# Performance work log

Measured on AMD Instinct MI355X. Metric: run time of the kernel, lower is better.

Reference implementation:

```python
import jax, jax.numpy as jnp
import numpy as np

N_NODES = 100000
N_EDGES = 1600000
D_IN = 64
D_HID = 64
D_OUT = 16


def setup_inputs() -> dict:
    key = jax.random.key(0)
    k1, k2, k3, k4 = jax.random.split(key, 4)
    x = jax.random.normal(k1, (N_NODES, D_IN), dtype=jnp.float32)
    edge_index = jax.random.randint(k2, (2, N_EDGES), 0, N_NODES, dtype=jnp.int64)
    # Glorot-ish scaled weights
    W1 = jax.random.normal(k3, (D_IN, D_HID), dtype=jnp.float32) / np.sqrt(D_IN)
    b1 = jnp.zeros((D_HID,), dtype=jnp.float32)
    W2 = jax.random.normal(k4, (D_HID, D_OUT), dtype=jnp.float32) / np.sqrt(D_HID)
    b2 = jnp.zeros((D_OUT,), dtype=jnp.float32)
    return {"x": x, "edge_index": edge_index, "W1": W1, "b1": b1, "W2": W2, "b2": b2}


def _gcn_conv(x, src, dst, W, b, n_nodes):
    """PyG GCNConv: D^{-1/2} (A + I) D^{-1/2} X W + b (self-loops added)."""
    h = x @ W  # [N, F_out]
    # degree including self-loop (counted on destination, PyG default)
    deg = jnp.zeros((n_nodes,), dtype=h.dtype).at[dst].add(1.0) + 1.0
    dinv = jax.lax.rsqrt(deg)  # deg >= 1, no inf
    # edge messages: norm_e = dinv[src] * dinv[dst]
    msg = h[src] * (dinv[src] * dinv[dst])[:, None]  # [E, F_out]
    out = jax.ops.segment_sum(msg, dst, num_segments=n_nodes)
    # self-loop contribution: norm = dinv[i]^2
    out = out + h * (dinv * dinv)[:, None]
    return out + b


def reference(x, edge_index, W1, b1, W2, b2):
    src, dst = edge_index[0], edge_index[1]
    n = x.shape[0]
    h = _gcn_conv(x, src, dst, W1, b1, n)
    h = jax.nn.relu(h)
    # F.dropout(training=False) at inference -> identity
    h = _gcn_conv(h, src, dst, W2, b2, n)
    return jax.nn.log_softmax(h, axis=1)
```

## Files before the change

kernel.cpp:

```cpp
#include <hip/hip_runtime.h>
#include <hip/hip_fp16.h>
#include <math.h>

#define N_NODES 100000
#define N_EDGES 1600000


__global__ void k_count(const int* __restrict__ dst, int* __restrict__ cnt,
                        unsigned short* __restrict__ rnk, int e) {
    int i = (blockIdx.x * blockDim.x + threadIdx.x) * 8;
    if (i + 8 <= e) {
        int4 dA = *(const int4*)(dst + i);
        int4 dB = *(const int4*)(dst + i + 4);
        int r0 = atomicAdd(&cnt[dA.x], 1);
        int r1 = atomicAdd(&cnt[dA.y], 1);
        int r2 = atomicAdd(&cnt[dA.z], 1);
        int r3 = atomicAdd(&cnt[dA.w], 1);
        int r4 = atomicAdd(&cnt[dB.x], 1);
        int r5 = atomicAdd(&cnt[dB.y], 1);
        int r6 = atomicAdd(&cnt[dB.z], 1);
        int r7 = atomicAdd(&cnt[dB.w], 1);
        int4 p;
        p.x = (r0 & 0xffff) | (r1 << 16);
        p.y = (r2 & 0xffff) | (r3 << 16);
        p.z = (r4 & 0xffff) | (r5 << 16);
        p.w = (r6 & 0xffff) | (r7 << 16);
        *(int4*)(rnk + i) = p;
    } else {
        for (; i < e; ++i) rnk[i] = (unsigned short)atomicAdd(&cnt[dst[i]], 1);
    }
}

__global__ void k_scanA(const int* __restrict__ cnt, int* __restrict__ off,
                        int* __restrict__ bsums, float* __restrict__ dinv, int n) {
    __shared__ int sd[256];
    int t = threadIdx.x;
    int base = blockIdx.x * 1024 + t * 4;
    int e0 = (base + 0 < n) ? cnt[base + 0] : 0;
    int e1 = (base + 1 < n) ? cnt[base + 1] : 0;
    int e2 = (base + 2 < n) ? cnt[base + 2] : 0;
    int e3 = (base + 3 < n) ? cnt[base + 3] : 0;
    if (base + 0 < n) dinv[base + 0] = rsqrtf((float)e0 + 1.0f);
    if (base + 1 < n) dinv[base + 1] = rsqrtf((float)e1 + 1.0f);
    if (base + 2 < n) dinv[base + 2] = rsqrtf((float)e2 + 1.0f);
    if (base + 3 < n) dinv[base + 3] = rsqrtf((float)e3 + 1.0f);
    int s = e0 + e1 + e2 + e3;
    sd[t] = s;
    __syncthreads();
    for (int o = 1; o < 256; o <<= 1) {
        int v = (t >= o) ? sd[t - o] : 0;
        __syncthreads();
        sd[t] += v;
        __syncthreads();
    }
    int excl = sd[t] - s;
    if (base + 0 < n) off[base + 0] = excl;
    if (base + 1 < n) off[base + 1] = excl + e0;
    if (base + 2 < n) off[base + 2] = excl + e0 + e1;
    if (base + 3 < n) off[base + 3] = excl + e0 + e1 + e2;
    if (t == 0) bsums[blockIdx.x] = sd[255];
}

__global__ void k_scanC(int* __restrict__ off, const int* __restrict__ bsums,
                        int nb, int n) {
    __shared__ int sd[128];
    int t = threadIdx.x;
    if (t < 128) sd[t] = (t < nb) ? bsums[t] : 0;
    __syncthreads();
    for (int o = 1; o < 128; o <<= 1) {
        int v = (t >= o && t < 128) ? sd[t - o] : 0;
        __syncthreads();
        if (t < 128) sd[t] += v;
        __syncthreads();
    }
    int i = blockIdx.x * 256 + t;
    if (i < n) {
        int b = i >> 10;
        int add = (b == 0) ? 0 : sd[b - 1];
        off[i] = off[i] + add;
    }
    if (blockIdx.x == 0 && t == 0) off[n] = sd[nb - 1];
}

__global__ void k_fill(const int* __restrict__ src, const int* __restrict__ dst,
                       const unsigned short* __restrict__ rnk,
                       const int* __restrict__ off, int* __restrict__ csr, int e) {
    int i = (blockIdx.x * blockDim.x + threadIdx.x) * 8;
    if (i + 8 <= e) {
        int4 sA = *(const int4*)(src + i), sB = *(const int4*)(src + i + 4);
        int4 dA = *(const int4*)(dst + i), dB = *(const int4*)(dst + i + 4);
        int4 rp = *(const int4*)(rnk + i);
        csr[off[dA.x] + (rp.x & 0xffff)] = sA.x;
        csr[off[dA.y] + ((unsigned)rp.x >> 16)] = sA.y;
        csr[off[dA.z] + (rp.y & 0xffff)] = sA.z;
        csr[off[dA.w] + ((unsigned)rp.y >> 16)] = sA.w;
        csr[off[dB.x] + (rp.z & 0xffff)] = sB.x;
        csr[off[dB.y] + ((unsigned)rp.z >> 16)] = sB.y;
        csr[off[dB.z] + (rp.w & 0xffff)] = sB.z;
        csr[off[dB.w] + ((unsigned)rp.w >> 16)] = sB.w;
    } else {
        for (; i < e; ++i) csr[off[dst[i]] + rnk[i]] = src[i];
    }
}

__global__ void k_fold(const float* __restrict__ x, const float* __restrict__ dinv,
                       float* __restrict__ xs) {
    int t = blockIdx.x * blockDim.x + threadIdx.x;
    float4 v = ((const float4*)x)[t];
    float di = dinv[t >> 4];
    float4 o;
    o.x = v.x * di; o.y = v.y * di; o.z = v.z * di; o.w = v.w * di;
    ((float4*)xs)[t] = o;
}


__global__ void k_agg1(
        const float* __restrict__ xs, const int* __restrict__ off,
        const int* __restrict__ csr, const float* __restrict__ dinv,
        const float* __restrict__ W1, const float* __restrict__ W2,
        const float* __restrict__ b1, __half* __restrict__ h2h, int n) {
    __shared__ float W1s[64 * 64];
    __shared__ float W2s[64 * 17];
    __shared__ float xsw[4][64];
    __shared__ float vsw[4][64];
    int tid = threadIdx.x;
    {
        const float4* W14 = (const float4*)W1;
        float4* W1s4 = (float4*)W1s;
#pragma unroll
        for (int i = 0; i < 4; ++i) W1s4[tid + 256 * i] = W14[tid + 256 * i];
        for (int i = tid; i < 64 * 16; i += 256) W2s[(i >> 4) * 17 + (i & 15)] = W2[i];
    }
    __syncthreads();

    int w = tid >> 6, lane = tid & 63;
    int f = lane;
    int G = lane >> 4;
    int c4 = lane & 15;
    float b1f = b1[f];

    int base = blockIdx.x * 16 + w * 4;
#pragma unroll 1
    for (int nn = 0; nn < 4; ++nn) {
        int d = base + nn;
        float dd = dinv[d];
        float a0 = xs[(size_t)d * 64 + f];
        float a1 = 0.f, a2 = 0.f, a3 = 0.f;
        int j = off[d], je = off[d + 1];
        int s0 = 0, s1 = 0, s2 = 0, s3 = 0;
        if (j + 4 <= je) { s0 = csr[j]; s1 = csr[j + 1]; s2 = csr[j + 2]; s3 = csr[j + 3]; }
        while (j + 4 <= je) {
            int t0 = s0, t1 = s1, t2 = s2, t3 = s3;
            if (j + 8 <= je) { t0 = csr[j + 4]; t1 = csr[j + 5]; t2 = csr[j + 6]; t3 = csr[j + 7]; }
            a0 += xs[(size_t)s0 * 64 + f];
            a1 += xs[(size_t)s1 * 64 + f];
            a2 += xs[(size_t)s2 * 64 + f];
            a3 += xs[(size_t)s3 * 64 + f];
            s0 = t0; s1 = t1; s2 = t2; s3 = t3;
            j += 4;
        }
        for (; j < je; ++j) {
            int s = csr[j];
            a0 += xs[(size_t)s * 64 + f];
        }
        xsw[w][f] = ((a0 + a1) + (a2 + a3)) * dd;
        float p0 = b1f, p1 = 0.f, p2 = 0.f, p3 = 0.f;
        const float4* xw4 = (const float4*)xsw[w];
#pragma unroll
        for (int k4 = 0; k4 < 16; ++k4) {
            float4 xv = xw4[k4];
            p0 = fmaf(xv.x, W1s[(k4 * 4 + 0) * 64 + f], p0);
            p1 = fmaf(xv.y, W1s[(k4 * 4 + 1) * 64 + f], p1);
            p2 = fmaf(xv.z, W1s[(k4 * 4 + 2) * 64 + f], p2);
            p3 = fmaf(xv.w, W1s[(k4 * 4 + 3) * 64 + f], p3);
        }
        vsw[w][f] = fmaxf((p0 + p1) + (p2 + p3), 0.f);
        float p = 0.f;
        const float4* vw4 = (const float4*)vsw[w];
#pragma unroll
        for (int kk4 = 0; kk4 < 4; ++kk4) {
            float4 vv = vw4[G * 4 + kk4];
            p = fmaf(vv.x, W2s[(G * 16 + kk4 * 4 + 0) * 17 + c4], p);
            p = fmaf(vv.y, W2s[(G * 16 + kk4 * 4 + 1) * 17 + c4], p);
            p = fmaf(vv.z, W2s[(G * 16 + kk4 * 4 + 2) * 17 + c4], p);
            p = fmaf(vv.w, W2s[(G * 16 + kk4 * 4 + 3) * 17 + c4], p);
        }
        p += __shfl_xor(p, 16);
        p += __shfl_xor(p, 32);
        if (G == 0) h2h[(size_t)d * 16 + c4] = __float2half(p * dd);
    }
}


__global__ void k_agg2_lsm(
        const __half* __restrict__ h2h, const int* __restrict__ off,
        const int* __restrict__ csr, const float* __restrict__ dinv,
        const float* __restrict__ b2, float* __restrict__ y, int n) {
    int tid = threadIdx.x;
    int w = tid >> 6, lane = tid & 63, g = lane >> 4, c = lane & 15;
    int d = blockIdx.x * 4 + w;
    float dd = dinv[d];
    float acc0 = (g == 0) ? __half2float(h2h[(size_t)d * 16 + c]) : 0.f;
    float acc1 = 0.f, acc2 = 0.f, acc3 = 0.f;
    int j = off[d], je = off[d + 1];
    for (; j + 16 <= je; j += 16) {
        int sA = csr[j + g], sB = csr[j + 4 + g];
        int sC = csr[j + 8 + g], sD = csr[j + 12 + g];
        acc0 += __half2float(h2h[(size_t)sA * 16 + c]);
        acc1 += __half2float(h2h[(size_t)sB * 16 + c]);
        acc2 += __half2float(h2h[(size_t)sC * 16 + c]);
        acc3 += __half2float(h2h[(size_t)sD * 16 + c]);
    }
    for (; j < je; j += 4) {
        if (j + g < je) {
            int s = csr[j + g];
            acc0 += __half2float(h2h[(size_t)s * 16 + c]);
        }
    }
    float acc = (acc0 + acc1) + (acc2 + acc3);
    acc += __shfl_xor(acc, 16);
    acc += __shfl_xor(acc, 32);
    float v = acc * dd + b2[c];
    float m = v;
#pragma unroll
    for (int o = 1; o < 16; o <<= 1) m = fmaxf(m, __shfl_xor(m, o));
    float ss = expf(v - m);
#pragma unroll
    for (int o = 1; o < 16; o <<= 1) ss += __shfl_xor(ss, o);
    float lse = logf(ss) + m;
    if (g == 0) y[(size_t)d * 16 + c] = v - lse;
}


extern "C" void kernel_launch(void* const* d_in, const int* in_sizes, int n_in,
                              void* d_out, int out_size, void* d_ws, size_t ws_size,
                              hipStream_t stream) {
    const float* x  = (const float*)d_in[0];
    const int*   ei = (const int*)d_in[1];
    const float* W1 = (const float*)d_in[2];
    const float* b1 = (const float*)d_in[3];
    const float* W2 = (const float*)d_in[4];
    const float* b2 = (const float*)d_in[5];
    float* y = (float*)d_out;

    const int n = N_NODES;
    const int e = N_EDGES;
    const int* src = ei;
    const int* dst = ei + e;

    float* ws = (float*)d_ws;
    int*            cnt   = (int*)ws;
    float*          dinv  = ws + 102400;
    int*            off   = (int*)(ws + 204800);
    int*            bsums = (int*)(ws + 307200);
    unsigned short* rnk   = (unsigned short*)(ws + 409600);
    int*            csr   = (int*)(ws + 1209600);
    float*          xs    = ws + 2809600;
    __half*         h2h   = (__half*)(ws + 9209600);

    const int nb = (n + 1023) / 1024;

    hipMemsetAsync(cnt, 0, (size_t)n * sizeof(int), stream);
    k_count<<<(e / 8 + 255) / 256, 256, 0, stream>>>(dst, cnt, rnk, e);
    k_scanA<<<nb, 256, 0, stream>>>(cnt, off, bsums, dinv, n);
    k_fold <<<n * 16 / 256, 256, 0, stream>>>(x, dinv, xs);
    k_scanC<<<(n + 255) / 256, 256, 0, stream>>>(off, bsums, nb, n);
    k_fill <<<(e / 8 + 255) / 256, 256, 0, stream>>>(src, dst, rnk, off, csr, e);

    k_agg1    <<<n / 16, 256, 0, stream>>>(xs, off, csr, dinv, W1, W2, b1, h2h, n);
    k_agg2_lsm<<<n / 4, 256, 0, stream>>>(h2h, off, csr, dinv, b2, y, n);
}
```

Baseline: 278.3 us.

## Fuse fold into fill kernel and vectorize layer-2 gather with half2

Merges the x-scaling fold kernel into the CSR fill kernel as extra blocks, recomputing dinv from the degree counts so it no longer depends on scanA's output. This removes one launch and lets the two independent memory-bound jobs run at the same time. The layer-2 aggregation now has each lane load half2 pairs with 8 lanes per row, so a wave processes 8 edges per step instead of 4. The output is also written as float2. Softmax shuffle reductions shrink to match the new lane layout.

```diff
diff --git a/kernel.cpp b/kernel.cpp
--- a/kernel.cpp
+++ b/kernel.cpp
@@ -82,35 +82,40 @@
     if (blockIdx.x == 0 && t == 0) off[n] = sd[nb - 1];
 }
 
-__global__ void k_fill(const int* __restrict__ src, const int* __restrict__ dst,
-                       const unsigned short* __restrict__ rnk,
-                       const int* __restrict__ off, int* __restrict__ csr, int e) {
-    int i = (blockIdx.x * blockDim.x + threadIdx.x) * 8;
-    if (i + 8 <= e) {
-        int4 sA = *(const int4*)(src + i), sB = *(const int4*)(src + i + 4);
-        int4 dA = *(const int4*)(dst + i), dB = *(const int4*)(dst + i + 4);
-        int4 rp = *(const int4*)(rnk + i);
-        csr[off[dA.x] + (rp.x & 0xffff)] = sA.x;
-        csr[off[dA.y] + ((unsigned)rp.x >> 16)] = sA.y;
-        csr[off[dA.z] + (rp.y & 0xffff)] = sA.z;
-        csr[off[dA.w] + ((unsigned)rp.y >> 16)] = sA.w;
-        csr[off[dB.x] + (rp.z & 0xffff)] = sB.x;
-        csr[off[dB.y] + ((unsigned)rp.z >> 16)] = sB.y;
-        csr[off[dB.z] + (rp.w & 0xffff)] = sB.z;
-        csr[off[dB.w] + ((unsigned)rp.w >> 16)] = sB.w;
+
+#define FILL_BLOCKS 782
+
+__global__ void k_fill_fold(const int* __restrict__ src, const int* __restrict__ dst,
+                            const unsigned short* __restrict__ rnk,
+                            const int* __restrict__ off, int* __restrict__ csr,
+                            const float* __restrict__ x, const int* __restrict__ cnt,
+                            float* __restrict__ xs, int e) {
+    int bid = blockIdx.x;
+    if (bid < FILL_BLOCKS) {
+        int i = (bid * blockDim.x + threadIdx.x) * 8;
+        if (i + 8 <= e) {
+            int4 sA = *(const int4*)(src + i), sB = *(const int4*)(src + i + 4);
+            int4 dA = *(const int4*)(dst + i), dB = *(const int4*)(dst + i + 4);
+            int4 rp = *(const int4*)(rnk + i);
+            csr[off[dA.x] + (rp.x & 0xffff)] = sA.x;
+            csr[off[dA.y] + ((unsigned)rp.x >> 16)] = sA.y;
+            csr[off[dA.z] + (rp.y & 0xffff)] = sA.z;
+            csr[off[dA.w] + ((unsigned)rp.y >> 16)] = sA.w;
+            csr[off[dB.x] + (rp.z & 0xffff)] = sB.x;
+            csr[off[dB.y] + ((unsigned)rp.z >> 16)] = sB.y;
+            csr[off[dB.z] + (rp.w & 0xffff)] = sB.z;
+            csr[off[dB.w] + ((unsigned)rp.w >> 16)] = sB.w;
+        } else {
+            for (; i < e; ++i) csr[off[dst[i]] + rnk[i]] = src[i];
+        }
     } else {
-        for (; i < e; ++i) csr[off[dst[i]] + rnk[i]] = src[i];
-    }
-}
-
-__global__ void k_fold(const float* __restrict__ x, const float* __restrict__ dinv,
-                       float* __restrict__ xs) {
-    int t = blockIdx.x * blockDim.x + threadIdx.x;
-    float4 v = ((const float4*)x)[t];
-    float di = dinv[t >> 4];
-    float4 o;
-    o.x = v.x * di; o.y = v.y * di; o.z = v.z * di; o.w = v.w * di;
-    ((float4*)xs)[t] = o;
+        int t = (bid - FILL_BLOCKS) * blockDim.x + threadIdx.x;
+        float4 v = ((const float4*)x)[t];
+        float di = rsqrtf((float)cnt[t >> 4] + 1.0f);
+        float4 o;
+        o.x = v.x * di; o.y = v.y * di; o.z = v.z * di; o.w = v.w * di;
+        ((float4*)xs)[t] = o;
+    }
 }
 
 
@@ -197,38 +202,47 @@
         const int* __restrict__ csr, const float* __restrict__ dinv,
         const float* __restrict__ b2, float* __restrict__ y, int n) {
     int tid = threadIdx.x;
-    int w = tid >> 6, lane = tid & 63, g = lane >> 4, c = lane & 15;
+    int w = tid >> 6, lane = tid & 63, g = lane >> 3, c2 = lane & 7;
     int d = blockIdx.x * 4 + w;
+    const __half2* h2 = (const __half2*)h2h;
     float dd = dinv[d];
-    float acc0 = (g == 0) ? __half2float(h2h[(size_t)d * 16 + c]) : 0.f;
-    float acc1 = 0.f, acc2 = 0.f, acc3 = 0.f;
+    float2 sv = __half22float2(h2[(size_t)d * 8 + c2]);
+    float ax0 = (g == 0) ? sv.x : 0.f;
+    float ay0 = (g == 0) ? sv.y : 0.f;
+    float ax1 = 0.f, ay1 = 0.f;
     int j = off[d], je = off[d + 1];
     for (; j + 16 <= je; j += 16) {
-        int sA = csr[j + g], sB = csr[j + 4 + g];
-        int sC = csr[j + 8 + g], sD = csr[j + 12 + g];
-        acc0 += __half2float(h2h[(size_t)sA * 16 + c]);
-        acc1 += __half2float(h2h[(size_t)sB * 16 + c]);
-        acc2 += __half2float(h2h[(size_t)sC * 16 + c]);
-        acc3 += __half2float(h2h[(size_t)sD * 16 + c]);
-    }
-    for (; j < je; j += 4) {
+        int sA = csr[j + g], sB = csr[j + 8 + g];
+        float2 vA = __half22float2(h2[(size_t)sA * 8 + c2]);
+        float2 vB = __half22float2(h2[(size_t)sB * 8 + c2]);
+        ax0 += vA.x; ay0 += vA.y;
+        ax1 += vB.x; ay1 += vB.y;
+    }
+    for (; j < je; j += 8) {
         if (j + g < je) {
             int s = csr[j + g];
-            acc0 += __half2float(h2h[(size_t)s * 16 + c]);
-        }
-    }
-    float acc = (acc0 + acc1) + (acc2 + acc3);
-    acc += __shfl_xor(acc, 16);
-    acc += __shfl_xor(acc, 32);
-    float v = acc * dd + b2[c];
-    float m = v;
-#pragma unroll
-    for (int o = 1; o < 16; o <<= 1) m = fmaxf(m, __shfl_xor(m, o));
-    float ss = expf(v - m);
-#pragma unroll
-    for (int o = 1; o < 16; o <<= 1) ss += __shfl_xor(ss, o);
+            float2 v = __half22float2(h2[(size_t)s * 8 + c2]);
+            ax0 += v.x; ay0 += v.y;
+        }
+    }
+    float ax = ax0 + ax1, ay = ay0 + ay1;
+    ax += __shfl_xor(ax, 8);  ax += __shfl_xor(ax, 16); ax += __shfl_xor(ax, 32);
+    ay += __shfl_xor(ay, 8);  ay += __shfl_xor(ay, 16); ay += __shfl_xor(ay, 32);
+    float vx = ax * dd + b2[c2 * 2 + 0];
+    float vy = ay * dd + b2[c2 * 2 + 1];
+    float m = fmaxf(vx, vy);
+    m = fmaxf(m, __shfl_xor(m, 1));
+    m = fmaxf(m, __shfl_xor(m, 2));
+    m = fmaxf(m, __shfl_xor(m, 4));
+    float ss = expf(vx - m) + expf(vy - m);
+    ss += __shfl_xor(ss, 1);
+    ss += __shfl_xor(ss, 2);
+    ss += __shfl_xor(ss, 4);
     float lse = logf(ss) + m;
-    if (g == 0) y[(size_t)d * 16 + c] = v - lse;
+    if (g == 0) {
+        float2 o; o.x = vx - lse; o.y = vy - lse;
+        ((float2*)y)[(size_t)d * 8 + c2] = o;
+    }
 }
 
 
@@ -263,10 +277,9 @@
     hipMemsetAsync(cnt, 0, (size_t)n * sizeof(int), stream);
     k_count<<<(e / 8 + 255) / 256, 256, 0, stream>>>(dst, cnt, rnk, e);
     k_scanA<<<nb, 256, 0, stream>>>(cnt, off, bsums, dinv, n);
-    k_fold <<<n * 16 / 256, 256, 0, stream>>>(x, dinv, xs);
     k_scanC<<<(n + 255) / 256, 256, 0, stream>>>(off, bsums, nb, n);
-    k_fill <<<(e / 8 + 255) / 256, 256, 0, stream>>>(src, dst, rnk, off, csr, e);
-
+    k_fill_fold<<<FILL_BLOCKS + n * 16 / 256, 256, 0, stream>>>(
+        src, dst, rnk, off, csr, x, cnt, xs, e);
     k_agg1    <<<n / 16, 256, 0, stream>>>(xs, off, csr, dinv, W1, W2, b1, h2h, n);
     k_agg2_lsm<<<n / 4, 256, 0, stream>>>(h2h, off, csr, dinv, b2, y, n);
 }
```

Measured after the change: 267.1 us. 1.04x faster.
